# Kernel tuning notes

Hardware: AMD Instinct MI355X
Metric: run time of the kernel (lower is better)

Reference implementation:

```python
import jax, jax.numpy as jnp
import numpy as np

N = 50000      # nodes
E = 800000     # edges
F_IN = 128     # input_dim
H = 4          # GAT heads
C = 32         # hidden_dim (per head)
HC = H * C     # 128, concat GAT output
NG = 64        # graphs in batch
OUT = 10       # classes


def _gat_conv(x, src, dst, W, att_src, att_dst, bias):
    # PyG GATConv (concat=True, add_self_loops=True, negative_slope=0.2)
    n = x.shape[0]
    h = (x @ W).reshape(n, H, -1)                      # [N,H,C]
    a_s = (h * att_src).sum(-1)                        # [N,H]
    a_d = (h * att_dst).sum(-1)                        # [N,H]
    loop = jnp.arange(n)
    s = jnp.concatenate([src, loop])                   # self-loops appended
    d = jnp.concatenate([dst, loop])
    e = jax.nn.leaky_relu(a_s[s] + a_d[d], 0.2)        # [E+N,H]
    m = jax.ops.segment_max(e, d, num_segments=n)
    e = jnp.exp(e - m[d])
    z = jax.ops.segment_sum(e, d, num_segments=n)
    alpha = e / (z[d] + 1e-16)                         # edge softmax per dst,head
    out = jax.ops.segment_sum(h[s] * alpha[..., None], d, num_segments=n)
    return out.reshape(n, -1) + bias                   # [N,H*C]


def setup_inputs() -> dict:
    key = jax.random.key(0)
    ks = jax.random.split(key, 20)
    g = lambda k, shp, fan: jax.random.normal(k, shp, jnp.float32) / np.sqrt(fan)
    inp = {
        'x': jax.random.normal(ks[0], (N, F_IN), jnp.float32),
        'edge_index': jax.random.randint(ks[1], (2, E), 0, N),
        'batch': jnp.sort(jax.random.randint(ks[2], (N,), 0, NG)),
        # GATConv 1: F_IN -> H*C
        'W1': g(ks[3], (F_IN, HC), F_IN),
        'as1': g(ks[4], (H, C), C), 'ad1': g(ks[5], (H, C), C),
        'b1': jnp.zeros((HC,), jnp.float32),
        # GATConv 2: H*C -> H*C
        'W2': g(ks[6], (HC, HC), HC),
        'as2': g(ks[7], (H, C), C), 'ad2': g(ks[8], (H, C), C),
        'b2': jnp.zeros((HC,), jnp.float32),
        # GraphConv: H*C -> C  (lin_rel has bias, lin_root does not)
        'W3r': g(ks[9], (HC, C), HC), 'W3l': g(ks[10], (HC, C), HC),
        'b3': jnp.zeros((C,), jnp.float32),
        # SAGEConv: C -> C (mean aggr; lin_l has bias, lin_r does not)
        'W4l': g(ks[11], (C, C), C), 'b4l': jnp.zeros((C,), jnp.float32),
        'W4r': g(ks[12], (C, C), C),
        # MLP head
        'Wf1': g(ks[13], (C, C), C), 'bf1': jnp.zeros((C,), jnp.float32),
        'Wf2': g(ks[14], (C, OUT), C), 'bf2': jnp.zeros((OUT,), jnp.float32),
    }
    return inp


def reference(x, edge_index, batch, W1, as1, ad1, b1, W2, as2, ad2, b2,
              W3r, W3l, b3, W4l, b4l, W4r, Wf1, bf1, Wf2, bf2):
    src, dst = edge_index[0], edge_index[1]
    relu = jax.nn.relu
    n = x.shape[0]
    # GAT layers (dropout is identity in eval)
    x = relu(_gat_conv(x, src, dst, W1, as1, ad1, b1))
    x = relu(_gat_conv(x, src, dst, W2, as2, ad2, b2))
    # GraphConv: lin_rel(sum_neighbors) + lin_root(x)
    agg = jax.ops.segment_sum(x[src], dst, num_segments=n)
    x = relu(agg @ W3r + b3 + x @ W3l)
    # SAGEConv: lin_l(mean_neighbors) + lin_r(x)
    deg = jax.ops.segment_sum(jnp.ones((src.shape[0],), x.dtype), dst, num_segments=n)
    mean = jax.ops.segment_sum(x[src], dst, num_segments=n) / jnp.maximum(deg, 1.0)[:, None]
    x = relu(mean @ W4l + b4l + x @ W4r)
    # global mean pool over graphs
    cnt = jax.ops.segment_sum(jnp.ones((n,), x.dtype), batch, num_segments=NG)
    gpool = jax.ops.segment_sum(x, batch, num_segments=NG) / jnp.maximum(cnt, 1.0)[:, None]
    gpool = relu(gpool @ Wf1 + bf1)
    return gpool @ Wf2 + bf2
```

## Files before the change

### kernel.cpp

```cpp
#include <hip/hip_runtime.h>
#include <hip/hip_bf16.h>
#include <type_traits>


typedef __bf16 v8bf __attribute__((ext_vector_type(8)));
typedef float  v4f  __attribute__((ext_vector_type(4)));

__device__ __forceinline__ float lrelu(float x) { return x > 0.f ? x : 0.2f * x; }

__device__ __forceinline__ unsigned short f2bf(float f) {
    unsigned u = __float_as_uint(f);
    unsigned r = (u + 0x7FFF + ((u >> 16) & 1)) >> 16;
    return (unsigned short)r;
}
__device__ __forceinline__ float bfbits2f(unsigned short u) {
    return __uint_as_float((unsigned)u << 16);
}
__device__ __forceinline__ float bflo(int v) { return __uint_as_float((unsigned)v << 16); }
__device__ __forceinline__ float bfhi(int v) { return __uint_as_float((unsigned)v & 0xffff0000u); }
__device__ __forceinline__ int packbf2(float a, float b) {
    return (int)f2bf(a) | ((int)f2bf(b) << 16);
}


__global__ __launch_bounds__(256) void bucket_hist(const int* __restrict__ dst,
                                                   int* __restrict__ bcount,
                                                   int E, int nbuck) {
    __shared__ int hist[256];
    int t = threadIdx.x;
    for (int i = t; i < nbuck; i += 256) hist[i] = 0;
    __syncthreads();
    int base = blockIdx.x * 4096;
    #pragma unroll
    for (int k = 0; k < 16; ++k) {
        int e = base + k * 256 + t;
        if (e < E) atomicAdd(&hist[dst[e] >> 8], 1);
    }
    __syncthreads();
    for (int i = t; i < nbuck; i += 256) {
        int c = hist[i];
        if (c) atomicAdd(&bcount[i], c);
    }
}

__global__ __launch_bounds__(256) void scan_convert(
    const int* __restrict__ bcount, int* __restrict__ bbase, int* __restrict__ gcursor,
    int nbuck, int E, int* __restrict__ rowptr, int n,
    const float* __restrict__ W1, const float* __restrict__ W2,
    const float* __restrict__ W3r, const float* __restrict__ W3l,
    const float* __restrict__ as1, const float* __restrict__ ad1,
    const float* __restrict__ as2, const float* __restrict__ ad2,
    __hip_bfloat16* __restrict__ W1t, __hip_bfloat16* __restrict__ W2t,
    __hip_bfloat16* __restrict__ W3rt, __hip_bfloat16* __restrict__ W3lt)
{
    int t = threadIdx.x;
    if (blockIdx.x == 0) {
        __shared__ int red[256];
        int v = (t < nbuck) ? bcount[t] : 0;
        red[t] = v;
        __syncthreads();
        for (int off = 1; off < 256; off <<= 1) {
            int u = (t >= off) ? red[t - off] : 0;
            __syncthreads();
            red[t] += u;
            __syncthreads();
        }
        int ex = red[t] - v;
        if (t < nbuck) { bbase[t] = ex; gcursor[t] = ex; }
        if (t == 0) { bbase[nbuck] = E; rowptr[n] = E; }
        return;
    }
    int b = blockIdx.x - 1;
    int i = b * 256 + t;
    {
        int k = i >> 7, c = i & 127;
        *(unsigned short*)&W1t[c * 128 + k] = f2bf(W1[i]);
        *(unsigned short*)&W2t[c * 128 + k] = f2bf(W2[i]);
    }
    if (i < 4096) {
        int k = i >> 5, c = i & 31;
        *(unsigned short*)&W3rt[c * 128 + k] = f2bf(W3r[i]);
        *(unsigned short*)&W3lt[c * 128 + k] = f2bf(W3l[i]);
    }
    if (b == 0) {
        for (int u = t; u < 512; u += 256) {
            int k = u & 127, hd = u >> 7;
            float vs1 = 0.f, vd1 = 0.f, vs2 = 0.f, vd2 = 0.f;
            #pragma unroll
            for (int j = 0; j < 32; ++j) {
                int c = hd * 32 + j;
                float w1 = W1[k * 128 + c], w2 = W2[k * 128 + c];
                vs1 += w1 * as1[c]; vd1 += w1 * ad1[c];
                vs2 += w2 * as2[c]; vd2 += w2 * ad2[c];
            }
            unsigned short h1s = f2bf(vs1), h1d = f2bf(vd1);
            unsigned short h2s = f2bf(vs2), h2d = f2bf(vd2);
            *(unsigned short*)&W1t[(128 + hd) * 128 + k] = h1s;
            *(unsigned short*)&W1t[(132 + hd) * 128 + k] = f2bf(vs1 - bfbits2f(h1s));
            *(unsigned short*)&W1t[(136 + hd) * 128 + k] = h1d;
            *(unsigned short*)&W1t[(140 + hd) * 128 + k] = f2bf(vd1 - bfbits2f(h1d));
            *(unsigned short*)&W2t[(128 + hd) * 128 + k] = h2s;
            *(unsigned short*)&W2t[(132 + hd) * 128 + k] = f2bf(vs2 - bfbits2f(h2s));
            *(unsigned short*)&W2t[(136 + hd) * 128 + k] = h2d;
            *(unsigned short*)&W2t[(140 + hd) * 128 + k] = f2bf(vd2 - bfbits2f(h2d));
        }
    }
}

__global__ __launch_bounds__(256) void bucket_scatter(const int* __restrict__ dst,
                                                      const int* __restrict__ src,
                                                      int* __restrict__ gcursor,
                                                      int* __restrict__ pairs,
                                                      int E, int nbuck) {
    __shared__ int hist[256], lcur[256];
    int t = threadIdx.x;
    for (int i = t; i < nbuck; i += 256) hist[i] = 0;
    __syncthreads();
    int base = blockIdx.x * 2048;
    int dreg[8];
    #pragma unroll
    for (int k = 0; k < 8; ++k) {
        int e = base + k * 256 + t;
        int d = (e < E) ? dst[e] : -1;
        dreg[k] = d;
        if (d >= 0) atomicAdd(&hist[d >> 8], 1);
    }
    __syncthreads();
    for (int i = t; i < nbuck; i += 256) {
        int c = hist[i];
        lcur[i] = c ? atomicAdd(&gcursor[i], c) : 0;
    }
    __syncthreads();
    #pragma unroll
    for (int k = 0; k < 8; ++k) {
        int e = base + k * 256 + t;
        if (e < E) {
            int d = dreg[k];
            int p = atomicAdd(&lcur[d >> 8], 1);
            pairs[p] = ((d & 255) << 17) | src[e];
        }
    }
}

__global__ __launch_bounds__(256) void bucket_fill(const int* __restrict__ pairs,
                                                   const int* __restrict__ bbase,
                                                   int* __restrict__ rowptr,
                                                   int* __restrict__ colsrc, int n) {
    __shared__ int deg[256], excl[256], cur[256];
    int b = blockIdx.x, t = threadIdx.x;
    int e0 = bbase[b], e1 = bbase[b + 1];
    int d0 = b << 8;
    deg[t] = 0;
    __syncthreads();
    for (int j = e0 + t; j < e1; j += 256)
        atomicAdd(&deg[pairs[j] >> 17], 1);
    __syncthreads();
    int v = deg[t];
    excl[t] = v;
    __syncthreads();
    for (int off = 1; off < 256; off <<= 1) {
        int u = (t >= off) ? excl[t - off] : 0;
        __syncthreads();
        excl[t] += u;
        __syncthreads();
    }
    int base = e0 + excl[t] - v;
    if (d0 + t < n) rowptr[d0 + t] = base;
    cur[t] = base;
    __syncthreads();
    for (int j = e0 + t; j < e1; j += 256) {
        int w = pairs[j];
        int p = atomicAdd(&cur[w >> 17], 1);
        colsrc[p] = w & 0x1FFFF;
    }
}

template <typename T>
__global__ __launch_bounds__(256) void gemm_att_mfma(
    const T* __restrict__ X, const __hip_bfloat16* __restrict__ Wt,
    __hip_bfloat16* __restrict__ h, float* __restrict__ a_s, float* __restrict__ a_d, int n)
{
    __shared__ __align__(16) __hip_bfloat16 sWt[144 * 136];
    int t = threadIdx.x;
    for (int i = t; i < 144 * 16; i += 256) {
        int row = i >> 4, ch = i & 15;
        *(int4*)&sWt[row * 136 + ch * 8] = *(const int4*)&Wt[row * 128 + ch * 8];
    }
    __syncthreads();
    int wave = t >> 6, lane = t & 63, quad = lane >> 4, l16 = lane & 15;
    int rowbase = (blockIdx.x * 4 + wave) * 16;
    if (rowbase >= n) return;

    v8bf z;
    #pragma unroll
    for (int i = 0; i < 8; ++i) z[i] = (__bf16)0.f;
    int arow = rowbase + l16;
    bool ok = arow < n;
    v8bf af[4];
    if constexpr (std::is_same<T, float>::value) {
        const float* xf = X + (size_t)(ok ? arow : 0) * 128;
        #pragma unroll
        for (int ks = 0; ks < 4; ++ks) {
            if (ok) {
                float4 u = *(const float4*)&xf[ks * 32 + quad * 8];
                float4 v = *(const float4*)&xf[ks * 32 + quad * 8 + 4];
                v8bf a;
                unsigned short r;
                r = f2bf(u.x); a[0] = *(__bf16*)&r;
                r = f2bf(u.y); a[1] = *(__bf16*)&r;
                r = f2bf(u.z); a[2] = *(__bf16*)&r;
                r = f2bf(u.w); a[3] = *(__bf16*)&r;
                r = f2bf(v.x); a[4] = *(__bf16*)&r;
                r = f2bf(v.y); a[5] = *(__bf16*)&r;
                r = f2bf(v.z); a[6] = *(__bf16*)&r;
                r = f2bf(v.w); a[7] = *(__bf16*)&r;
                af[ks] = a;
            } else af[ks] = z;
        }
    } else {
        const v8bf* px = (const v8bf*)(X + (size_t)(ok ? arow : 0) * 128);
        #pragma unroll
        for (int ks = 0; ks < 4; ++ks) af[ks] = ok ? px[ks * 4 + quad] : z;
    }

    v4f acc[9];
    #pragma unroll
    for (int ct = 0; ct < 9; ++ct) acc[ct] = (v4f){0.f, 0.f, 0.f, 0.f};
    #pragma unroll
    for (int ct = 0; ct < 9; ++ct) {
        #pragma unroll
        for (int ks = 0; ks < 4; ++ks) {
            v8bf b = *(const v8bf*)&sWt[(ct * 16 + l16) * 136 + ks * 32 + quad * 8];
            acc[ct] = __builtin_amdgcn_mfma_f32_16x16x32_bf16(af[ks], b, acc[ct], 0, 0, 0);
        }
    }

    #pragma unroll
    for (int reg = 0; reg < 4; ++reg) {
        int r = rowbase + quad * 4 + reg;
        if (r < n) {
            #pragma unroll
            for (int ct = 0; ct < 8; ++ct)
                *(unsigned short*)&h[(size_t)r * 128 + ct * 16 + l16] = f2bf(acc[ct][reg]);
        }
    }
    #pragma unroll
    for (int reg = 0; reg < 4; ++reg) {
        float v = acc[8][reg] + __shfl_xor(acc[8][reg], 4);
        int r = rowbase + quad * 4 + reg;
        if (r < n) {
            if (l16 < 4)                    a_s[r * 4 + l16] = v;
            else if (l16 >= 8 && l16 < 12)  a_d[r * 4 + (l16 - 8)] = v;
        }
    }
}

__global__ __launch_bounds__(256) void gat_aggr(
    const __hip_bfloat16* __restrict__ h, const float* __restrict__ a_s,
    const float* __restrict__ a_d,
    const int* __restrict__ rowptr, const int* __restrict__ colsrc,
    const float* __restrict__ bias, __hip_bfloat16* __restrict__ out, int n)
{
    __shared__ float s_w[4][64 * 4];
    int t = threadIdx.x;
    int wave = t >> 6, lane = t & 63;
    int d = blockIdx.x * 4 + wave;
    if (d >= n) d = n - 1;
    int beg = rowptr[d], end = rowptr[d + 1];
    int cnt = end - beg;
    float4 ad4 = *(const float4*)&a_d[d * 4];
    float4 asd = *(const float4*)&a_s[d * 4];
    float es0 = lrelu(asd.x + ad4.x), es1 = lrelu(asd.y + ad4.y);
    float es2 = lrelu(asd.z + ad4.z), es3 = lrelu(asd.w + ad4.w);
    float z0 = 0.f, z1 = 0.f, z2 = 0.f, z3 = 0.f;

    int l16 = lane & 15, egrp = lane >> 4;
    int ch = l16 * 8;
    int head = l16 >> 2;
    float acc[8];
    #pragma unroll
    for (int i = 0; i < 8; ++i) acc[i] = 0.f;

    for (int j0 = 0; j0 < cnt; j0 += 64) {
        int ne = min(64, cnt - j0);
        float w0 = 0.f, w1 = 0.f, w2 = 0.f, w3 = 0.f;
        int s = 0;
        if (lane < ne) {
            s = colsrc[beg + j0 + lane];
            float4 sv = *(const float4*)&a_s[s * 4];
            w0 = __expf(lrelu(sv.x + ad4.x));
            w1 = __expf(lrelu(sv.y + ad4.y));
            w2 = __expf(lrelu(sv.z + ad4.z));
            w3 = __expf(lrelu(sv.w + ad4.w));
        }
        z0 += w0; z1 += w1; z2 += w2; z3 += w3;
        float4 wv = {w0, w1, w2, w3};
        *(float4*)&s_w[wave][lane * 4] = wv;
        __asm volatile("s_waitcnt lgkmcnt(0)" ::: "memory");
        int kmax = (ne + 3) >> 2;
        #pragma unroll 2
        for (int k = 0; k < kmax; ++k) {
            int j = egrp + 4 * k;
            int ss = __shfl(s, j);
            float wj = s_w[wave][j * 4 + head];
            int4 u = *(const int4*)&h[(size_t)ss * 128 + ch];
            acc[0] += wj * bflo(u.x); acc[1] += wj * bfhi(u.x);
            acc[2] += wj * bflo(u.y); acc[3] += wj * bfhi(u.y);
            acc[4] += wj * bflo(u.z); acc[5] += wj * bfhi(u.z);
            acc[6] += wj * bflo(u.w); acc[7] += wj * bfhi(u.w);
        }
    }
    #pragma unroll
    for (int off = 1; off < 64; off <<= 1) {
        z0 += __shfl_xor(z0, off);
        z1 += __shfl_xor(z1, off);
        z2 += __shfl_xor(z2, off);
        z3 += __shfl_xor(z3, off);
    }
    #pragma unroll
    for (int off = 16; off < 64; off <<= 1)
        #pragma unroll
        for (int i = 0; i < 8; ++i) acc[i] += __shfl_xor(acc[i], off);

    if (egrp == 0) {
        float zh = (head < 2) ? (head == 0 ? z0 : z1) : (head == 2 ? z2 : z3);
        float eh = (head < 2) ? (head == 0 ? es0 : es1) : (head == 2 ? es2 : es3);
        float ws = __expf(eh);
        float inv = 1.f / (zh + ws + 1e-16f);
        int4 hu = *(const int4*)&h[(size_t)d * 128 + ch];
        float hs[8] = {bflo(hu.x), bfhi(hu.x), bflo(hu.y), bfhi(hu.y),
                       bflo(hu.z), bfhi(hu.z), bflo(hu.w), bfhi(hu.w)};
        float4 b0 = *(const float4*)&bias[ch];
        float4 b1 = *(const float4*)&bias[ch + 4];
        float o[8];
        o[0] = fmaxf((acc[0] + ws * hs[0]) * inv + b0.x, 0.f);
        o[1] = fmaxf((acc[1] + ws * hs[1]) * inv + b0.y, 0.f);
        o[2] = fmaxf((acc[2] + ws * hs[2]) * inv + b0.z, 0.f);
        o[3] = fmaxf((acc[3] + ws * hs[3]) * inv + b0.w, 0.f);
        o[4] = fmaxf((acc[4] + ws * hs[4]) * inv + b1.x, 0.f);
        o[5] = fmaxf((acc[5] + ws * hs[5]) * inv + b1.y, 0.f);
        o[6] = fmaxf((acc[6] + ws * hs[6]) * inv + b1.z, 0.f);
        o[7] = fmaxf((acc[7] + ws * hs[7]) * inv + b1.w, 0.f);
        int4 ou;
        ou.x = packbf2(o[0], o[1]); ou.y = packbf2(o[2], o[3]);
        ou.z = packbf2(o[4], o[5]); ou.w = packbf2(o[6], o[7]);
        *(int4*)&out[(size_t)d * 128 + ch] = ou;
    }
}

__global__ __launch_bounds__(256) void graphconv_lin(
    const __hip_bfloat16* __restrict__ Xb,
    const __hip_bfloat16* __restrict__ Wrt, const __hip_bfloat16* __restrict__ Wlt,
    const float* __restrict__ bias, __hip_bfloat16* __restrict__ y,
    float* __restrict__ root, int n)
{
    __shared__ __align__(16) __hip_bfloat16 sWr[32 * 136], sWl[32 * 136];
    int t = threadIdx.x;
    for (int i = t; i < 32 * 16; i += 256) {
        int row = i >> 4, ch = i & 15;
        *(int4*)&sWr[row * 136 + ch * 8] = *(const int4*)&Wrt[row * 128 + ch * 8];
        *(int4*)&sWl[row * 136 + ch * 8] = *(const int4*)&Wlt[row * 128 + ch * 8];
    }
    __syncthreads();
    int wave = t >> 6, lane = t & 63, quad = lane >> 4, l16 = lane & 15;
    int rowbase = (blockIdx.x * 4 + wave) * 16;
    if (rowbase >= n) return;

    v8bf z;
    #pragma unroll
    for (int i = 0; i < 8; ++i) z[i] = (__bf16)0.f;
    int arow = rowbase + l16;
    bool ok = arow < n;
    const v8bf* px = (const v8bf*)(Xb + (size_t)(ok ? arow : 0) * 128);
    v8bf fx[4];
    #pragma unroll
    for (int ks = 0; ks < 4; ++ks) fx[ks] = ok ? px[ks * 4 + quad] : z;

    v4f accR[2], accL[2];
    #pragma unroll
    for (int ct = 0; ct < 2; ++ct) {
        accR[ct] = (v4f){0.f, 0.f, 0.f, 0.f};
        accL[ct] = (v4f){0.f, 0.f, 0.f, 0.f};
        #pragma unroll
        for (int ks = 0; ks < 4; ++ks) {
            v8bf br = *(const v8bf*)&sWr[(ct * 16 + l16) * 136 + ks * 32 + quad * 8];
            accR[ct] = __builtin_amdgcn_mfma_f32_16x16x32_bf16(fx[ks], br, accR[ct], 0, 0, 0);
            v8bf bl = *(const v8bf*)&sWl[(ct * 16 + l16) * 136 + ks * 32 + quad * 8];
            accL[ct] = __builtin_amdgcn_mfma_f32_16x16x32_bf16(fx[ks], bl, accL[ct], 0, 0, 0);
        }
    }
    #pragma unroll
    for (int ct = 0; ct < 2; ++ct) {
        float bcol = bias[ct * 16 + l16];
        #pragma unroll
        for (int reg = 0; reg < 4; ++reg) {
            int r = rowbase + quad * 4 + reg;
            if (r < n) {
                *(unsigned short*)&y[(size_t)r * 32 + ct * 16 + l16] = f2bf(accR[ct][reg]);
                root[(size_t)r * 32 + ct * 16 + l16] = accL[ct][reg] + bcol;
            }
        }
    }
}

__global__ __launch_bounds__(256) void graphconv_aggr(
    const __hip_bfloat16* __restrict__ y, const float* __restrict__ root,
    const int* __restrict__ rowptr, const int* __restrict__ colsrc,
    __hip_bfloat16* __restrict__ x3, int n)
{
    int t = threadIdx.x;
    int wave = t >> 6, lane = t & 63;
    int d = blockIdx.x * 4 + wave;
    if (d >= n) d = n - 1;
    int beg = rowptr[d], end = rowptr[d + 1];
    int cnt = end - beg;
    int l4 = lane & 3, egrp = lane >> 2;
    int ch = l4 * 8;
    float acc[8];
    #pragma unroll
    for (int i = 0; i < 8; ++i) acc[i] = 0.f;
    for (int j0 = 0; j0 < cnt; j0 += 64) {
        int ne = min(64, cnt - j0);
        int s = (lane < ne) ? colsrc[beg + j0 + lane] : 0;
        int kmax = (ne + 15) >> 4;
        #pragma unroll 2
        for (int k = 0; k < kmax; ++k) {
            int j = egrp + 16 * k;
            int ss = __shfl(s, j);
            float m = (j < ne) ? 1.f : 0.f;
            int4 u = *(const int4*)&y[(size_t)ss * 32 + ch];
            acc[0] += m * bflo(u.x); acc[1] += m * bfhi(u.x);
            acc[2] += m * bflo(u.y); acc[3] += m * bfhi(u.y);
            acc[4] += m * bflo(u.z); acc[5] += m * bfhi(u.z);
            acc[6] += m * bflo(u.w); acc[7] += m * bfhi(u.w);
        }
    }
    #pragma unroll
    for (int off = 4; off < 64; off <<= 1)
        #pragma unroll
        for (int i = 0; i < 8; ++i) acc[i] += __shfl_xor(acc[i], off);
    if (egrp == 0) {
        float4 r0 = *(const float4*)&root[(size_t)d * 32 + ch];
        float4 r1 = *(const float4*)&root[(size_t)d * 32 + ch + 4];
        float o[8];
        o[0] = fmaxf(acc[0] + r0.x, 0.f); o[1] = fmaxf(acc[1] + r0.y, 0.f);
        o[2] = fmaxf(acc[2] + r0.z, 0.f); o[3] = fmaxf(acc[3] + r0.w, 0.f);
        o[4] = fmaxf(acc[4] + r1.x, 0.f); o[5] = fmaxf(acc[5] + r1.y, 0.f);
        o[6] = fmaxf(acc[6] + r1.z, 0.f); o[7] = fmaxf(acc[7] + r1.w, 0.f);
        int4 ou;
        ou.x = packbf2(o[0], o[1]); ou.y = packbf2(o[2], o[3]);
        ou.z = packbf2(o[4], o[5]); ou.w = packbf2(o[6], o[7]);
        *(int4*)&x3[(size_t)d * 32 + ch] = ou;
    }
}

__global__ __launch_bounds__(256) void mean_aggr32(
    const __hip_bfloat16* __restrict__ x, const int* __restrict__ rowptr,
    const int* __restrict__ colsrc, float* __restrict__ mean, int n)
{
    int t = threadIdx.x;
    int wave = t >> 6, lane = t & 63;
    int d = blockIdx.x * 4 + wave;
    if (d >= n) d = n - 1;
    int beg = rowptr[d], end = rowptr[d + 1];
    int cnt = end - beg;
    int l4 = lane & 3, egrp = lane >> 2;
    int ch = l4 * 8;
    float acc[8];
    #pragma unroll
    for (int i = 0; i < 8; ++i) acc[i] = 0.f;
    for (int j0 = 0; j0 < cnt; j0 += 64) {
        int ne = min(64, cnt - j0);
        int s = (lane < ne) ? colsrc[beg + j0 + lane] : 0;
        int kmax = (ne + 15) >> 4;
        #pragma unroll 2
        for (int k = 0; k < kmax; ++k) {
            int j = egrp + 16 * k;
            int ss = __shfl(s, j);
            float m = (j < ne) ? 1.f : 0.f;
            int4 u = *(const int4*)&x[(size_t)ss * 32 + ch];
            acc[0] += m * bflo(u.x); acc[1] += m * bfhi(u.x);
            acc[2] += m * bflo(u.y); acc[3] += m * bfhi(u.y);
            acc[4] += m * bflo(u.z); acc[5] += m * bfhi(u.z);
            acc[6] += m * bflo(u.w); acc[7] += m * bfhi(u.w);
        }
    }
    #pragma unroll
    for (int off = 4; off < 64; off <<= 1)
        #pragma unroll
        for (int i = 0; i < 8; ++i) acc[i] += __shfl_xor(acc[i], off);
    if (egrp == 0) {
        float invd = 1.f / fmaxf((float)cnt, 1.f);
        float4 lo = {acc[0] * invd, acc[1] * invd, acc[2] * invd, acc[3] * invd};
        float4 hi = {acc[4] * invd, acc[5] * invd, acc[6] * invd, acc[7] * invd};
        *(float4*)&mean[(size_t)d * 32 + ch]     = lo;
        *(float4*)&mean[(size_t)d * 32 + ch + 4] = hi;
    }
}

__global__ __launch_bounds__(256) void sage_gemm(
    const float* __restrict__ mean, const __hip_bfloat16* __restrict__ xin,
    const float* __restrict__ Wl, const float* __restrict__ bl,
    const float* __restrict__ Wr, float* __restrict__ out, int n)
{
    __shared__ __align__(16) float sWl[32 * 32], sWr[32 * 32];
    __shared__ __align__(16) float sm[8 * 32], sx[8 * 32];
    int t = threadIdx.x;
    for (int i = t; i < 1024; i += 256) { sWl[i] = Wl[i]; sWr[i] = Wr[i]; }
    int c = t & 31, rr = t >> 5;
    float bc = bl[c];
    for (int row0 = blockIdx.x * 8; row0 < n; row0 += gridDim.x * 8) {
        __syncthreads();
        {
            int i = t;
            int r = i >> 5, cc = i & 31;
            int row = row0 + r;
            sm[i] = (row < n) ? mean[row * 32 + cc] : 0.f;
            sx[i] = (row < n) ? bfbits2f(*(const unsigned short*)&xin[row * 32 + cc]) : 0.f;
        }
        __syncthreads();
        float acc = bc;
        const float4* pm = (const float4*)&sm[rr * 32];
        const float4* px = (const float4*)&sx[rr * 32];
        #pragma unroll
        for (int k4 = 0; k4 < 8; ++k4) {
            float4 vm = pm[k4], vx = px[k4];
            const float* wl = &sWl[(k4 * 4) * 32 + c];
            const float* wr = &sWr[(k4 * 4) * 32 + c];
            acc += vm.x * wl[0] + vm.y * wl[32] + vm.z * wl[64] + vm.w * wl[96];
            acc += vx.x * wr[0] + vx.y * wr[32] + vx.z * wr[64] + vx.w * wr[96];
        }
        int row = row0 + rr;
        if (row < n) out[row * 32 + c] = fmaxf(acc, 0.f);
    }
}

__device__ __forceinline__ int lower_bound_i(const int* a, int n, int key) {
    int lo = 0, hi = n;
    while (lo < hi) { int mid = (lo + hi) >> 1; if (a[mid] < key) lo = mid + 1; else hi = mid; }
    return lo;
}

__global__ __launch_bounds__(256) void pool_kernel(
    const float* __restrict__ x, const int* __restrict__ batch,
    float* __restrict__ gpool, int n)
{
    int g = blockIdx.x;
    int lo = lower_bound_i(batch, n, g);
    int hi = lower_bound_i(batch, n, g + 1);
    int t = threadIdx.x;
    int c = t & 31, rr = t >> 5;
    float acc = 0.f;
    for (int i = lo + rr; i < hi; i += 8) acc += x[i * 32 + c];
    __shared__ float sred[256];
    sred[t] = acc;
    __syncthreads();
    if (t < 128) sred[t] += sred[t + 128];
    __syncthreads();
    if (t < 64) sred[t] += sred[t + 64];
    __syncthreads();
    if (t < 32) {
        float v = sred[t] + sred[t + 32];
        gpool[g * 32 + t] = v / fmaxf((float)(hi - lo), 1.f);
    }
}

__global__ __launch_bounds__(256) void head_kernel(
    const float* __restrict__ gpool, const float* __restrict__ Wf1, const float* __restrict__ bf1,
    const float* __restrict__ Wf2, const float* __restrict__ bf2, float* __restrict__ out)
{
    __shared__ float sg[64 * 32], st[64 * 32];
    __shared__ float sW1[32 * 32], sW2[32 * 10];
    int t = threadIdx.x;
    for (int i = t; i < 2048; i += 256) sg[i] = gpool[i];
    for (int i = t; i < 1024; i += 256) sW1[i] = Wf1[i];
    for (int i = t; i < 320; i += 256) sW2[i] = Wf2[i];
    __syncthreads();
    for (int i = t; i < 2048; i += 256) {
        int g = i >> 5, c = i & 31;
        float acc = bf1[c];
        #pragma unroll
        for (int k = 0; k < 32; ++k) acc += sg[g * 32 + k] * sW1[k * 32 + c];
        st[i] = fmaxf(acc, 0.f);
    }
    __syncthreads();
    for (int i = t; i < 640; i += 256) {
        int g = i / 10, o = i - g * 10;
        float acc = bf2[o];
        #pragma unroll
        for (int k = 0; k < 32; ++k) acc += st[g * 32 + k] * sW2[k * 10 + o];
        out[i] = acc;
    }
}

extern "C" void kernel_launch(void* const* d_in, const int* in_sizes, int n_in,
                              void* d_out, int out_size, void* d_ws, size_t ws_size,
                              hipStream_t stream) {
    const float* x    = (const float*)d_in[0];
    const int*   ei   = (const int*)d_in[1];
    const int*   batch= (const int*)d_in[2];
    const float* W1   = (const float*)d_in[3];
    const float* as1  = (const float*)d_in[4];
    const float* ad1  = (const float*)d_in[5];
    const float* b1   = (const float*)d_in[6];
    const float* W2   = (const float*)d_in[7];
    const float* as2  = (const float*)d_in[8];
    const float* ad2  = (const float*)d_in[9];
    const float* b2   = (const float*)d_in[10];
    const float* W3r  = (const float*)d_in[11];
    const float* W3l  = (const float*)d_in[12];
    const float* b3   = (const float*)d_in[13];
    const float* W4l  = (const float*)d_in[14];
    const float* b4l  = (const float*)d_in[15];
    const float* W4r  = (const float*)d_in[16];
    const float* Wf1  = (const float*)d_in[17];
    const float* bf1  = (const float*)d_in[18];
    const float* Wf2  = (const float*)d_in[19];
    const float* bf2  = (const float*)d_in[20];

    const int N = in_sizes[0] / 128;
    const int E = in_sizes[1] / 2;
    const int* src = ei;
    const int* dst = ei + E;

    char* p = (char*)d_ws;
    auto alloc = [&](size_t bytes) -> void* {
        void* r = (void*)p;
        p += (bytes + 255) & ~(size_t)255;
        return r;
    };
    __hip_bfloat16* buf1 = (__hip_bfloat16*)alloc((size_t)N * 128 * 2);
    __hip_bfloat16* buf2 = (__hip_bfloat16*)alloc((size_t)N * 128 * 2);
    __hip_bfloat16* buf3 = (__hip_bfloat16*)alloc((size_t)N * 128 * 2);
    float* aS     = (float*)alloc((size_t)N * 4 * 4);
    float* aD     = (float*)alloc((size_t)N * 4 * 4);
    int*   rowptr = (int*)alloc((size_t)(N + 1) * 4);
    int*   colsrc = (int*)alloc((size_t)E * 4);
    int*   bcount = (int*)alloc(256 * 4);
    int*   bbase  = (int*)alloc(257 * 4);
    int*   gcursor= (int*)alloc(256 * 4);
    __hip_bfloat16* W1t  = (__hip_bfloat16*)alloc(144 * 128 * 2);
    __hip_bfloat16* W2t  = (__hip_bfloat16*)alloc(144 * 128 * 2);
    __hip_bfloat16* W3rt = (__hip_bfloat16*)alloc(32 * 128 * 2);
    __hip_bfloat16* W3lt = (__hip_bfloat16*)alloc(32 * 128 * 2);
    float* gpool  = (float*)alloc(64 * 32 * 4);

    __hip_bfloat16* X3b  = buf2;
    float*          MEAN = (float*)((char*)buf2 + (((size_t)N * 32 * 2 + 255) & ~(size_t)255));
    float*          X4   = (float*)buf1;
    __hip_bfloat16* Y32  = buf3;
    float*          ROOT = (float*)((char*)buf3 + (((size_t)N * 32 * 2 + 255) & ~(size_t)255));
    int*            pairs = (int*)buf3;

    const int nbuck = (N + 255) >> 8;

    hipMemsetAsync(bcount, 0, 256 * 4, stream);
    bucket_hist<<<(E + 4095) / 4096, 256, 0, stream>>>(dst, bcount, E, nbuck);
    scan_convert<<<65, 256, 0, stream>>>(bcount, bbase, gcursor, nbuck, E, rowptr, N,
                                         W1, W2, W3r, W3l, as1, ad1, as2, ad2,
                                         W1t, W2t, W3rt, W3lt);
    bucket_scatter<<<(E + 2047) / 2048, 256, 0, stream>>>(dst, src, gcursor, pairs, E, nbuck);
    bucket_fill<<<nbuck, 256, 0, stream>>>(pairs, bbase, rowptr, colsrc, N);

    const int gmm = (N + 63) / 64;
    const int gag = (N + 3) / 4;
    gemm_att_mfma<float><<<gmm, 256, 0, stream>>>(x, W1t, buf3, aS, aD, N);
    gat_aggr<<<gag, 256, 0, stream>>>(buf3, aS, aD, rowptr, colsrc, b1, buf2, N);
    gemm_att_mfma<__hip_bfloat16><<<gmm, 256, 0, stream>>>(buf2, W2t, buf3, aS, aD, N);
    gat_aggr<<<gag, 256, 0, stream>>>(buf3, aS, aD, rowptr, colsrc, b2, buf1, N);
    graphconv_lin<<<gmm, 256, 0, stream>>>(buf1, W3rt, W3lt, b3, Y32, ROOT, N);
    graphconv_aggr<<<gag, 256, 0, stream>>>(Y32, ROOT, rowptr, colsrc, X3b, N);
    mean_aggr32<<<gag, 256, 0, stream>>>(X3b, rowptr, colsrc, MEAN, N);
    sage_gemm<<<1024, 256, 0, stream>>>(MEAN, X3b, W4l, b4l, W4r, X4, N);
    pool_kernel<<<64, 256, 0, stream>>>(X4, batch, gpool, N);
    head_kernel<<<1, 256, 0, stream>>>(gpool, Wf1, bf1, Wf2, bf2, (float*)d_out);
}
```

Measured before the change: 359.3 us.

## Persistent grid for MFMA GEMMs and unrolled gathers in GAT aggregation

Caps the GEMM kernels at 320 blocks and turns them into grid-stride loops, so each block loads the transposed weight tile into shared memory once and reuses it across many 16-row tiles. The GAT aggregation loop is unrolled by four with all gather loads issued before the FMAs, uses 32-bit byte-offset addressing, and keeps a single per-head softmax denominator partial per lane instead of four full-wave reductions. Self-feature, bias and root loads are moved ahead of the shuffle reductions to hide their latency. The cost is fewer resident blocks for the GEMMs and somewhat higher register pressure in the aggregation kernel.

New measurement: 356.2 us. About the same (-0.9%).

```diff
diff --git a/kernel.cpp b/kernel.cpp
--- a/kernel.cpp
+++ b/kernel.cpp
@@ -20,6 +20,13 @@
 __device__ __forceinline__ float bfhi(int v) { return __uint_as_float((unsigned)v & 0xffff0000u); }
 __device__ __forceinline__ int packbf2(float a, float b) {
     return (int)f2bf(a) | ((int)f2bf(b) << 16);
+}
+
+__device__ __forceinline__ void fma8(float* acc, int4 u, float w) {
+    acc[0] += w * bflo(u.x); acc[1] += w * bfhi(u.x);
+    acc[2] += w * bflo(u.y); acc[3] += w * bfhi(u.y);
+    acc[4] += w * bflo(u.z); acc[5] += w * bfhi(u.z);
+    acc[6] += w * bflo(u.w); acc[7] += w * bfhi(u.w);
 }
 
 
@@ -183,74 +190,77 @@
     __shared__ __align__(16) __hip_bfloat16 sWt[144 * 136];
     int t = threadIdx.x;
     for (int i = t; i < 144 * 16; i += 256) {
-        int row = i >> 4, ch = i & 15;
-        *(int4*)&sWt[row * 136 + ch * 8] = *(const int4*)&Wt[row * 128 + ch * 8];
+        int row = i >> 4, chh = i & 15;
+        *(int4*)&sWt[row * 136 + chh * 8] = *(const int4*)&Wt[row * 128 + chh * 8];
     }
     __syncthreads();
     int wave = t >> 6, lane = t & 63, quad = lane >> 4, l16 = lane & 15;
-    int rowbase = (blockIdx.x * 4 + wave) * 16;
-    if (rowbase >= n) return;
 
     v8bf z;
     #pragma unroll
     for (int i = 0; i < 8; ++i) z[i] = (__bf16)0.f;
-    int arow = rowbase + l16;
-    bool ok = arow < n;
-    v8bf af[4];
-    if constexpr (std::is_same<T, float>::value) {
-        const float* xf = X + (size_t)(ok ? arow : 0) * 128;
-        #pragma unroll
-        for (int ks = 0; ks < 4; ++ks) {
-            if (ok) {
-                float4 u = *(const float4*)&xf[ks * 32 + quad * 8];
-                float4 v = *(const float4*)&xf[ks * 32 + quad * 8 + 4];
-                v8bf a;
-                unsigned short r;
-                r = f2bf(u.x); a[0] = *(__bf16*)&r;
-                r = f2bf(u.y); a[1] = *(__bf16*)&r;
-                r = f2bf(u.z); a[2] = *(__bf16*)&r;
-                r = f2bf(u.w); a[3] = *(__bf16*)&r;
-                r = f2bf(v.x); a[4] = *(__bf16*)&r;
-                r = f2bf(v.y); a[5] = *(__bf16*)&r;
-                r = f2bf(v.z); a[6] = *(__bf16*)&r;
-                r = f2bf(v.w); a[7] = *(__bf16*)&r;
-                af[ks] = a;
-            } else af[ks] = z;
-        }
-    } else {
-        const v8bf* px = (const v8bf*)(X + (size_t)(ok ? arow : 0) * 128);
-        #pragma unroll
-        for (int ks = 0; ks < 4; ++ks) af[ks] = ok ? px[ks * 4 + quad] : z;
-    }
-
-    v4f acc[9];
-    #pragma unroll
-    for (int ct = 0; ct < 9; ++ct) acc[ct] = (v4f){0.f, 0.f, 0.f, 0.f};
-    #pragma unroll
-    for (int ct = 0; ct < 9; ++ct) {
-        #pragma unroll
-        for (int ks = 0; ks < 4; ++ks) {
-            v8bf b = *(const v8bf*)&sWt[(ct * 16 + l16) * 136 + ks * 32 + quad * 8];
-            acc[ct] = __builtin_amdgcn_mfma_f32_16x16x32_bf16(af[ks], b, acc[ct], 0, 0, 0);
-        }
-    }
-
-    #pragma unroll
-    for (int reg = 0; reg < 4; ++reg) {
-        int r = rowbase + quad * 4 + reg;
-        if (r < n) {
+
+    int nrb = (n + 15) >> 4;
+    for (int rb = blockIdx.x * 4 + wave; rb < nrb; rb += gridDim.x * 4) {
+        int rowbase = rb * 16;
+        int arow = rowbase + l16;
+        bool ok = arow < n;
+        v8bf af[4];
+        if constexpr (std::is_same<T, float>::value) {
+            const float* xf = X + (size_t)(ok ? arow : 0) * 128;
             #pragma unroll
-            for (int ct = 0; ct < 8; ++ct)
-                *(unsigned short*)&h[(size_t)r * 128 + ct * 16 + l16] = f2bf(acc[ct][reg]);
-        }
-    }
-    #pragma unroll
-    for (int reg = 0; reg < 4; ++reg) {
-        float v = acc[8][reg] + __shfl_xor(acc[8][reg], 4);
-        int r = rowbase + quad * 4 + reg;
-        if (r < n) {
-            if (l16 < 4)                    a_s[r * 4 + l16] = v;
-            else if (l16 >= 8 && l16 < 12)  a_d[r * 4 + (l16 - 8)] = v;
+            for (int ks = 0; ks < 4; ++ks) {
+                if (ok) {
+                    float4 u = *(const float4*)&xf[ks * 32 + quad * 8];
+                    float4 v = *(const float4*)&xf[ks * 32 + quad * 8 + 4];
+                    v8bf a;
+                    unsigned short r;
+                    r = f2bf(u.x); a[0] = *(__bf16*)&r;
+                    r = f2bf(u.y); a[1] = *(__bf16*)&r;
+                    r = f2bf(u.z); a[2] = *(__bf16*)&r;
+                    r = f2bf(u.w); a[3] = *(__bf16*)&r;
+                    r = f2bf(v.x); a[4] = *(__bf16*)&r;
+                    r = f2bf(v.y); a[5] = *(__bf16*)&r;
+                    r = f2bf(v.z); a[6] = *(__bf16*)&r;
+                    r = f2bf(v.w); a[7] = *(__bf16*)&r;
+                    af[ks] = a;
+                } else af[ks] = z;
+            }
+        } else {
+            const v8bf* px = (const v8bf*)(X + (size_t)(ok ? arow : 0) * 128);
+            #pragma unroll
+            for (int ks = 0; ks < 4; ++ks) af[ks] = ok ? px[ks * 4 + quad] : z;
+        }
+
+        v4f acc[9];
+        #pragma unroll
+        for (int ct = 0; ct < 9; ++ct) acc[ct] = (v4f){0.f, 0.f, 0.f, 0.f};
+        #pragma unroll
+        for (int ct = 0; ct < 9; ++ct) {
+            #pragma unroll
+            for (int ks = 0; ks < 4; ++ks) {
+                v8bf b = *(const v8bf*)&sWt[(ct * 16 + l16) * 136 + ks * 32 + quad * 8];
+                acc[ct] = __builtin_amdgcn_mfma_f32_16x16x32_bf16(af[ks], b, acc[ct], 0, 0, 0);
+            }
+        }
+
+        #pragma unroll
+        for (int reg = 0; reg < 4; ++reg) {
+            int r = rowbase + quad * 4 + reg;
+            if (r < n) {
+                #pragma unroll
+                for (int ct = 0; ct < 8; ++ct)
+                    *(unsigned short*)&h[(size_t)r * 128 + ct * 16 + l16] = f2bf(acc[ct][reg]);
+            }
+        }
+        #pragma unroll
+        for (int reg = 0; reg < 4; ++reg) {
+            float v = acc[8][reg] + __shfl_xor(acc[8][reg], 4);
+            int r = rowbase + quad * 4 + reg;
+            if (r < n) {
+                if (l16 < 4)                    a_s[r * 4 + l16] = v;
+                else if (l16 >= 8 && l16 < 12)  a_d[r * 4 + (l16 - 8)] = v;
+            }
         }
     }
 }
@@ -272,14 +282,17 @@
     float4 asd = *(const float4*)&a_s[d * 4];
     float es0 = lrelu(asd.x + ad4.x), es1 = lrelu(asd.y + ad4.y);
     float es2 = lrelu(asd.z + ad4.z), es3 = lrelu(asd.w + ad4.w);
-    float z0 = 0.f, z1 = 0.f, z2 = 0.f, z3 = 0.f;
 
     int l16 = lane & 15, egrp = lane >> 4;
     int ch = l16 * 8;
     int head = l16 >> 2;
+    const char* hb = (const char*)h;
+    unsigned chb = (unsigned)(ch << 1);
+
     float acc[8];
     #pragma unroll
     for (int i = 0; i < 8; ++i) acc[i] = 0.f;
+    float zp = 0.f;
 
     for (int j0 = 0; j0 < cnt; j0 += 64) {
         int ne = min(64, cnt - j0);
@@ -293,45 +306,73 @@
             w2 = __expf(lrelu(sv.z + ad4.z));
             w3 = __expf(lrelu(sv.w + ad4.w));
         }
-        z0 += w0; z1 += w1; z2 += w2; z3 += w3;
         float4 wv = {w0, w1, w2, w3};
         *(float4*)&s_w[wave][lane * 4] = wv;
         __asm volatile("s_waitcnt lgkmcnt(0)" ::: "memory");
         int kmax = (ne + 3) >> 2;
-        #pragma unroll 2
-        for (int k = 0; k < kmax; ++k) {
-            int j = egrp + 4 * k;
-            int ss = __shfl(s, j);
-            float wj = s_w[wave][j * 4 + head];
-            int4 u = *(const int4*)&h[(size_t)ss * 128 + ch];
-            acc[0] += wj * bflo(u.x); acc[1] += wj * bfhi(u.x);
-            acc[2] += wj * bflo(u.y); acc[3] += wj * bfhi(u.y);
-            acc[4] += wj * bflo(u.z); acc[5] += wj * bfhi(u.z);
-            acc[6] += wj * bflo(u.w); acc[7] += wj * bfhi(u.w);
-        }
-    }
-    #pragma unroll
-    for (int off = 1; off < 64; off <<= 1) {
-        z0 += __shfl_xor(z0, off);
-        z1 += __shfl_xor(z1, off);
-        z2 += __shfl_xor(z2, off);
-        z3 += __shfl_xor(z3, off);
-    }
-    #pragma unroll
-    for (int off = 16; off < 64; off <<= 1)
+        int k = 0;
+        for (; k + 4 <= kmax; k += 4) {
+            int jb = egrp + 4 * k;
+            int ss0 = __shfl(s, jb);
+            int ss1 = __shfl(s, jb + 4);
+            int ss2 = __shfl(s, jb + 8);
+            int ss3 = __shfl(s, jb + 12);
+            float wj0 = s_w[wave][jb * 4 + head];
+            float wj1 = s_w[wave][(jb + 4) * 4 + head];
+            float wj2 = s_w[wave][(jb + 8) * 4 + head];
+            float wj3 = s_w[wave][(jb + 12) * 4 + head];
+            int4 u0 = *(const int4*)(hb + (((unsigned)ss0 << 8) + chb));
+            int4 u1 = *(const int4*)(hb + (((unsigned)ss1 << 8) + chb));
+            int4 u2 = *(const int4*)(hb + (((unsigned)ss2 << 8) + chb));
+            int4 u3 = *(const int4*)(hb + (((unsigned)ss3 << 8) + chb));
+            zp += (wj0 + wj1) + (wj2 + wj3);
+            fma8(acc, u0, wj0);
+            fma8(acc, u1, wj1);
+            fma8(acc, u2, wj2);
+            fma8(acc, u3, wj3);
+        }
+        for (; k + 2 <= kmax; k += 2) {
+            int jb = egrp + 4 * k;
+            int ss0 = __shfl(s, jb);
+            int ss1 = __shfl(s, jb + 4);
+            float wj0 = s_w[wave][jb * 4 + head];
+            float wj1 = s_w[wave][(jb + 4) * 4 + head];
+            int4 u0 = *(const int4*)(hb + (((unsigned)ss0 << 8) + chb));
+            int4 u1 = *(const int4*)(hb + (((unsigned)ss1 << 8) + chb));
+            zp += wj0 + wj1;
+            fma8(acc, u0, wj0);
+            fma8(acc, u1, wj1);
+        }
+        if (k < kmax) {
+            int jb = egrp + 4 * k;
+            int ss0 = __shfl(s, jb);
+            float wj0 = s_w[wave][jb * 4 + head];
+            int4 u0 = *(const int4*)(hb + (((unsigned)ss0 << 8) + chb));
+            zp += wj0;
+            fma8(acc, u0, wj0);
+        }
+    }
+
+    int4 hu = {0, 0, 0, 0};
+    float4 b0 = {0.f, 0.f, 0.f, 0.f}, b1 = {0.f, 0.f, 0.f, 0.f};
+    if (egrp == 0) {
+        hu = *(const int4*)(hb + (((unsigned)d << 8) + chb));
+        b0 = *(const float4*)&bias[ch];
+        b1 = *(const float4*)&bias[ch + 4];
+    }
+    #pragma unroll
+    for (int off = 16; off < 64; off <<= 1) {
+        zp += __shfl_xor(zp, off);
         #pragma unroll
         for (int i = 0; i < 8; ++i) acc[i] += __shfl_xor(acc[i], off);
+    }
 
     if (egrp == 0) {
-        float zh = (head < 2) ? (head == 0 ? z0 : z1) : (head == 2 ? z2 : z3);
         float eh = (head < 2) ? (head == 0 ? es0 : es1) : (head == 2 ? es2 : es3);
         float ws = __expf(eh);
-        float inv = 1.f / (zh + ws + 1e-16f);
-        int4 hu = *(const int4*)&h[(size_t)d * 128 + ch];
+        float inv = 1.f / (zp + ws + 1e-16f);
         float hs[8] = {bflo(hu.x), bfhi(hu.x), bflo(hu.y), bfhi(hu.y),
                        bflo(hu.z), bfhi(hu.z), bflo(hu.w), bfhi(hu.w)};
-        float4 b0 = *(const float4*)&bias[ch];
-        float4 b1 = *(const float4*)&bias[ch + 4];
         float o[8];
         o[0] = fmaxf((acc[0] + ws * hs[0]) * inv + b0.x, 0.f);
         o[1] = fmaxf((acc[1] + ws * hs[1]) * inv + b0.y, 0.f);
@@ -357,47 +398,50 @@
     __shared__ __align__(16) __hip_bfloat16 sWr[32 * 136], sWl[32 * 136];
     int t = threadIdx.x;
     for (int i = t; i < 32 * 16; i += 256) {
-        int row = i >> 4, ch = i & 15;
-        *(int4*)&sWr[row * 136 + ch * 8] = *(const int4*)&Wrt[row * 128 + ch * 8];
-        *(int4*)&sWl[row * 136 + ch * 8] = *(const int4*)&Wlt[row * 128 + ch * 8];
+        int row = i >> 4, chh = i & 15;
+        *(int4*)&sWr[row * 136 + chh * 8] = *(const int4*)&Wrt[row * 128 + chh * 8];
+        *(int4*)&sWl[row * 136 + chh * 8] = *(const int4*)&Wlt[row * 128 + chh * 8];
     }
     __syncthreads();
     int wave = t >> 6, lane = t & 63, quad = lane >> 4, l16 = lane & 15;
-    int rowbase = (blockIdx.x * 4 + wave) * 16;
-    if (rowbase >= n) return;
 
     v8bf z;
     #pragma unroll
     for (int i = 0; i < 8; ++i) z[i] = (__bf16)0.f;
-    int arow = rowbase + l16;
-    bool ok = arow < n;
-    const v8bf* px = (const v8bf*)(Xb + (size_t)(ok ? arow : 0) * 128);
-    v8bf fx[4];
-    #pragma unroll
-    for (int ks = 0; ks < 4; ++ks) fx[ks] = ok ? px[ks * 4 + quad] : z;
-
-    v4f accR[2], accL[2];
-    #pragma unroll
-    for (int ct = 0; ct < 2; ++ct) {
-        accR[ct] = (v4f){0.f, 0.f, 0.f, 0.f};
-        accL[ct] = (v4f){0.f, 0.f, 0.f, 0.f};
-        #pragma unroll
-        for (int ks = 0; ks < 4; ++ks) {
-            v8bf br = *(const v8bf*)&sWr[(ct * 16 + l16) * 136 + ks * 32 + quad * 8];
-            accR[ct] = __builtin_amdgcn_mfma_f32_16x16x32_bf16(fx[ks], br, accR[ct], 0, 0, 0);
-            v8bf bl = *(const v8bf*)&sWl[(ct * 16 + l16) * 136 + ks * 32 + quad * 8];
-            accL[ct] = __builtin_amdgcn_mfma_f32_16x16x32_bf16(fx[ks], bl, accL[ct], 0, 0, 0);
-        }
-    }
-    #pragma unroll
-    for (int ct = 0; ct < 2; ++ct) {
-        float bcol = bias[ct * 16 + l16];
-        #pragma unroll
-        for (int reg = 0; reg < 4; ++reg) {
-            int r = rowbase + quad * 4 + reg;
-            if (r < n) {
-                *(unsigned short*)&y[(size_t)r * 32 + ct * 16 + l16] = f2bf(accR[ct][reg]);
-                root[(size_t)r * 32 + ct * 16 + l16] = accL[ct][reg] + bcol;
+
+    int nrb = (n + 15) >> 4;
+    for (int rb = blockIdx.x * 4 + wave; rb < nrb; rb += gridDim.x * 4) {
+        int rowbase = rb * 16;
+        int arow = rowbase + l16;
+        bool ok = arow < n;
+        const v8bf* px = (const v8bf*)(Xb + (size_t)(ok ? arow : 0) * 128);
+        v8bf fx[4];
+        #pragma unroll
+        for (int ks = 0; ks < 4; ++ks) fx[ks] = ok ? px[ks * 4 + quad] : z;
+
+        v4f accR[2], accL[2];
+        #pragma unroll
+        for (int ct = 0; ct < 2; ++ct) {
+            accR[ct] = (v4f){0.f, 0.f, 0.f, 0.f};
+            accL[ct] = (v4f){0.f, 0.f, 0.f, 0.f};
+            #pragma unroll
+            for (int ks = 0; ks < 4; ++ks) {
+                v8bf br = *(const v8bf*)&sWr[(ct * 16 + l16) * 136 + ks * 32 + quad * 8];
+                accR[ct] = __builtin_amdgcn_mfma_f32_16x16x32_bf16(fx[ks], br, accR[ct], 0, 0, 0);
+                v8bf bl = *(const v8bf*)&sWl[(ct * 16 + l16) * 136 + ks * 32 + quad * 8];
+                accL[ct] = __builtin_amdgcn_mfma_f32_16x16x32_bf16(fx[ks], bl, accL[ct], 0, 0, 0);
+            }
+        }
+        #pragma unroll
+        for (int ct = 0; ct < 2; ++ct) {
+            float bcol = bias[ct * 16 + l16];
+            #pragma unroll
+            for (int reg = 0; reg < 4; ++reg) {
+                int r = rowbase + quad * 4 + reg;
+                if (r < n) {
+                    *(unsigned short*)&y[(size_t)r * 32 + ct * 16 + l16] = f2bf(accR[ct][reg]);
+                    root[(size_t)r * 32 + ct * 16 + l16] = accL[ct][reg] + bcol;
+                }
             }
         }
     }
@@ -435,13 +479,16 @@
             acc[6] += m * bflo(u.w); acc[7] += m * bfhi(u.w);
         }
     }
+    float4 r0 = {0.f, 0.f, 0.f, 0.f}, r1 = {0.f, 0.f, 0.f, 0.f};
+    if (egrp == 0) {
+        r0 = *(const float4*)&root[(size_t)d * 32 + ch];
+        r1 = *(const float4*)&root[(size_t)d * 32 + ch + 4];
+    }
     #pragma unroll
     for (int off = 4; off < 64; off <<= 1)
         #pragma unroll
         for (int i = 0; i < 8; ++i) acc[i] += __shfl_xor(acc[i], off);
     if (egrp == 0) {
-        float4 r0 = *(const float4*)&root[(size_t)d * 32 + ch];
-        float4 r1 = *(const float4*)&root[(size_t)d * 32 + ch + 4];
         float o[8];
         o[0] = fmaxf(acc[0] + r0.x, 0.f); o[1] = fmaxf(acc[1] + r0.y, 0.f);
         o[2] = fmaxf(acc[2] + r0.z, 0.f); o[3] = fmaxf(acc[3] + r0.w, 0.f);
@@ -662,7 +709,8 @@
     bucket_scatter<<<(E + 2047) / 2048, 256, 0, stream>>>(dst, src, gcursor, pairs, E, nbuck);
     bucket_fill<<<nbuck, 256, 0, stream>>>(pairs, bbase, rowptr, colsrc, N);
 
-    const int gmm = (N + 63) / 64;
+    int gmm = (N + 63) / 64;
+    if (gmm > 320) gmm = 320;
     const int gag = (N + 3) / 4;
     gemm_att_mfma<float><<<gmm, 256, 0, stream>>>(x, W1t, buf3, aS, aD, N);
     gat_aggr<<<gag, 256, 0, stream>>>(buf3, aS, aD, rowptr, colsrc, b1, buf2, N);
```
